# Performance work log

Measured on AMD Instinct MI355X. Metric: run time of the kernel, lower is better.

Reference implementation:

```python
import jax, jax.numpy as jnp
import numpy as np
from jax import lax

NSTEPS = 7
BN_EPS = 1e-5


def setup_inputs() -> dict:
    key = jax.random.key(0)
    ks = jax.random.split(key, 7)
    bs, in_ch, h, w, k = 8, 16, 256, 256, 3
    f = jax.random.normal(ks[0], (bs, in_ch, h, w), dtype=jnp.float32)
    vec_w = jax.random.normal(ks[1], (2 * in_ch, in_ch, k, k), dtype=jnp.float32) * 0.1
    vec_b = jax.random.normal(ks[2], (2 * in_ch,), dtype=jnp.float32) * 0.1
    bn_gamma = jnp.ones((2 * in_ch,), dtype=jnp.float32)
    bn_beta = jnp.zeros((2 * in_ch,), dtype=jnp.float32)
    fuse_w = jax.random.normal(ks[3], (in_ch, in_ch, NSTEPS, 1, 1), dtype=jnp.float32) * 0.1
    fuse_b = jax.random.normal(ks[4], (in_ch,), dtype=jnp.float32) * 0.1
    return {"f": f, "vec_w": vec_w, "vec_b": vec_b, "bn_gamma": bn_gamma,
            "bn_beta": bn_beta, "fuse_w": fuse_w, "fuse_b": fuse_b}


def _bilinear_sample(src, py, px):
    """Bilinear sample with zero padding (torch grid_sample align_corners=True).
    src: [N,C,H,W]; py,px: [N,H,W] pixel coordinates (row, col)."""
    N, C, H, W = src.shape
    y0 = jnp.floor(py); x0 = jnp.floor(px)
    wy1 = py - y0; wy0 = 1.0 - wy1
    wx1 = px - x0; wx0 = 1.0 - wx1
    src_flat = src.reshape(N, C, H * W)

    def gather(yi, xi):
        valid = (yi >= 0) & (yi <= H - 1) & (xi >= 0) & (xi <= W - 1)
        yc = jnp.clip(yi, 0, H - 1).astype(jnp.int32)
        xc = jnp.clip(xi, 0, W - 1).astype(jnp.int32)
        idx = (yc * W + xc).reshape(N, 1, H * W)
        vals = jnp.take_along_axis(src_flat, idx, axis=2).reshape(N, C, H, W)
        return vals * valid.astype(src.dtype)[:, None, :, :]

    out = (wy0 * wx0)[:, None] * gather(y0, x0) \
        + (wy0 * wx1)[:, None] * gather(y0, x0 + 1) \
        + (wy1 * wx0)[:, None] * gather(y0 + 1, x0) \
        + (wy1 * wx1)[:, None] * gather(y0 + 1, x0 + 1)
    return out


def _warp(src, flow, grid_y, grid_x):
    # grid + flow in pixel space; original normalizes to [-1,1] then grid_sample
    # un-normalizes with align_corners=True, which is exactly pixel coords grid+flow.
    py = grid_y[None] + flow[:, 0]
    px = grid_x[None] + flow[:, 1]
    return _bilinear_sample(src, py, px)


def reference(f, vec_w, vec_b, bn_gamma, bn_beta, fuse_w, fuse_b):
    bs, in_ch, h, w = f.shape
    # vec_conv + BatchNorm2d (training-mode batch stats, biased variance)
    vec = lax.conv_general_dilated(f, vec_w, (1, 1), [(1, 1), (1, 1)],
                                   dimension_numbers=("NCHW", "OIHW", "NCHW"))
    vec = vec + vec_b[None, :, None, None]
    mean = vec.mean(axis=(0, 2, 3))
    var = vec.var(axis=(0, 2, 3))
    vec = bn_gamma[None, :, None, None] * (vec - mean[None, :, None, None]) \
        * lax.rsqrt(var + BN_EPS)[None, :, None, None] + bn_beta[None, :, None, None]

    c = vec.shape[1]  # = 2*in_ch
    vec = vec.reshape(bs * c // 2, 2, h, w)  # per-channel 2D flow fields

    grid_y, grid_x = jnp.meshgrid(jnp.arange(h, dtype=f.dtype),
                                  jnp.arange(w, dtype=f.dtype), indexing="ij")

    # VecInt: scaling and squaring, keeping every intermediate deformation
    vec = vec * (1.0 / 2 ** NSTEPS)
    deforms = []
    for _ in range(NSTEPS):
        vec = vec + _warp(vec, vec, grid_y, grid_x)
        deforms.append(vec)

    fsrc = f.reshape(bs * in_ch, 1, h, w)
    maps = [_warp(fsrc, d, grid_y, grid_x).reshape(bs, in_ch, h, w) for d in deforms]
    stacked = jnp.stack(maps, axis=2)  # [bs, in_ch, nsteps, h, w]

    # Conv3d with kernel (nsteps,1,1) then squeeze -> per-pixel channel/step mix
    out = jnp.einsum("ocs,bcshw->bohw", fuse_w[:, :, :, 0, 0], stacked)
    out = out + fuse_b[None, :, None, None]
    return out
```

## Files before the change

### kernel.cpp

```cpp
#include <hip/hip_runtime.h>
#include <hip/hip_fp16.h>

#define H 256
#define W 256
#define BS 8
#define IC 16
#define OCH 32
#define NSTEPS 7
#define PLANE (H*W)
#define NFIELDS (BS*IC)
#define BN_N (BS*PLANE)
#define BN_EPS 1e-5f
#define PW 260
#define PSZ (260 * 260)

__global__ void transpose_w_kernel(const float* __restrict__ w,
                                   __half2* __restrict__ wTh) {
    for (int idx = threadIdx.x; idx < IC * 9 * 16; idx += blockDim.x) {
        int rc = idx >> 4;
        int p  = idx & 15;
        float lo = w[(2 * p) * (IC * 9) + rc];
        float hi = w[(2 * p + 1) * (IC * 9) + rc];
        wTh[idx] = __floats2half2_rn(lo, hi);
    }
}

__global__ void guard_zero_kernel(unsigned* __restrict__ bufA,
                                  unsigned* __restrict__ bufB,
                                  unsigned short* __restrict__ f16p) {
    int p = blockIdx.x;
    size_t pb = (size_t)p * PSZ;
    for (int i = threadIdx.x; i < 2064; i += blockDim.x) {
        int row, col;
        if (i < 1040) {
            int r = i / 260;
            row = (r == 0) ? 0 : 256 + r;
            col = i - r * 260;
        } else {
            int j = i - 1040;
            int c = j / 256;
            col = (c == 0) ? 0 : 256 + c;
            row = 1 + (j - c * 256);
        }
        size_t off = pb + (size_t)row * PW + col;
        bufA[off] = 0u;
        bufB[off] = 0u;
        f16p[off] = 0;
    }
}

__global__ __launch_bounds__(256) void dup_kernel(const float* __restrict__ f,
                                                  __half* __restrict__ f16p) {
    int blk = blockIdx.x;
    int p  = blk >> 3;
    int r0 = (blk & 7) * 32;
    const float* fp = f + (size_t)p * PLANE;
    __half* dp = f16p + (size_t)p * PSZ;
    int tx = threadIdx.x;
#pragma unroll 4
    for (int ry = 0; ry < 32; ++ry) {
        int y = r0 + ry;
        dp[(size_t)(y + 1) * PW + tx + 1] = __float2half(fp[(size_t)y * W + tx]);
    }
}

__global__ __launch_bounds__(256, 8) void conv_kernel(
    const float* __restrict__ f, const __half2* __restrict__ wTh,
    const float* __restrict__ vec_b, __half2* __restrict__ vec_out) {
    __shared__ __align__(16) __half sf[16][10][40];

    int blk = blockIdx.x;
    int xcd = blk & 7;
    int i   = blk >> 3;
    int b   = i >> 5;
    int j   = i & 31;
    int ty0 = ((xcd << 2) | (j >> 3)) * 8;
    int tx0 = (j & 7) * 32;
    int tid = threadIdx.x;

    {
        int sic = tid >> 4;
        int st  = tid & 15;
        if (st < 10) {
            int gx0 = tx0 - 4 + 4 * st;
            const float* fpl = f + (size_t)(b * IC + sic) * PLANE;
            bool full = (gx0 >= 0) && (gx0 + 3 < W);
#pragma unroll
            for (int r = 0; r < 10; ++r) {
                int gy = ty0 - 1 + r;
                float4 v = make_float4(0.f, 0.f, 0.f, 0.f);
                if ((unsigned)gy < (unsigned)H) {
                    if (full) {
                        v = *(const float4*)(fpl + (size_t)gy * W + gx0);
                    } else {
                        if ((unsigned)(gx0 + 0) < (unsigned)W) v.x = fpl[(size_t)gy * W + gx0 + 0];
                        if ((unsigned)(gx0 + 1) < (unsigned)W) v.y = fpl[(size_t)gy * W + gx0 + 1];
                        if ((unsigned)(gx0 + 2) < (unsigned)W) v.z = fpl[(size_t)gy * W + gx0 + 2];
                        if ((unsigned)(gx0 + 3) < (unsigned)W) v.w = fpl[(size_t)gy * W + gx0 + 3];
                    }
                }
                union { __half2 h[2]; float2 f2; } u;
                u.h[0] = __floats2half2_rn(v.x, v.y);
                u.h[1] = __floats2half2_rn(v.z, v.w);
                *(float2*)&sf[sic][r][4 * st] = u.f2;
            }
        }
    }

    __half2 acc[16];
#pragma unroll
    for (int p = 0; p < 16; ++p)
        acc[p] = __floats2half2_rn(vec_b[2 * p], vec_b[2 * p + 1]);

    __syncthreads();

    int tyl = tid >> 5, txl = tid & 31;
#pragma unroll 2
    for (int ic = 0; ic < 16; ++ic) {
#pragma unroll
        for (int k = 0; k < 9; ++k) {
            int ky = k / 3, kx = k - ky * 3;
            __half2 fv = __half2half2(sf[ic][tyl + ky][txl + kx + 3]);
            const __half2* wrow = wTh + (ic * 9 + k) * 16;
#pragma unroll
            for (int p = 0; p < 16; ++p)
                acc[p] = __hfma2(fv, wrow[p], acc[p]);
        }
    }

    int y = ty0 + tyl, x = tx0 + txl;
#pragma unroll
    for (int c = 0; c < IC; ++c)
        vec_out[(size_t)(b * IC + c) * PLANE + (size_t)y * W + x] = acc[c];
}

__global__ __launch_bounds__(256) void stats_kernel(
    const __half2* __restrict__ vec, float* __restrict__ stats) {
    int blk   = blockIdx.x;
    int n     = blk >> 4;
    int chunk = blk & 15;
    const float4* p4 = (const float4*)(vec + (size_t)n * PLANE + chunk * 4096);
    int tid = threadIdx.x;

    float s0 = 0.f, s1 = 0.f, q0 = 0.f, q1 = 0.f;
#pragma unroll 2
    for (int i = tid; i < 1024; i += 256) {
        float4 w = p4[i];
        const __half2* hh = (const __half2*)&w;
#pragma unroll
        for (int q = 0; q < 4; ++q) {
            float2 v = __half22float2(hh[q]);
            s0 += v.x; s1 += v.y;
            q0 = fmaf(v.x, v.x, q0);
            q1 = fmaf(v.y, v.y, q1);
        }
    }
#pragma unroll
    for (int off = 32; off > 0; off >>= 1) {
        s0 += __shfl_down(s0, off, 64);
        s1 += __shfl_down(s1, off, 64);
        q0 += __shfl_down(q0, off, 64);
        q1 += __shfl_down(q1, off, 64);
    }
    __shared__ float red[4][4];
    int wave = tid >> 6, lane = tid & 63;
    if (lane == 0) {
        red[wave][0] = s0; red[wave][1] = s1;
        red[wave][2] = q0; red[wave][3] = q1;
    }
    __syncthreads();
    if (tid == 0) {
        float t0 = 0.f, t1 = 0.f, t2 = 0.f, t3 = 0.f;
#pragma unroll
        for (int wv = 0; wv < 4; ++wv) {
            t0 += red[wv][0]; t1 += red[wv][1];
            t2 += red[wv][2]; t3 += red[wv][3];
        }
        int ch0 = 2 * (n & 15);
        atomicAdd(stats + ch0,          t0);
        atomicAdd(stats + ch0 + 1,      t1);
        atomicAdd(stats + 32 + ch0,     t2);
        atomicAdd(stats + 32 + ch0 + 1, t3);
    }
}

__global__ void finalize_kernel(const float* __restrict__ stats,
                                const float* __restrict__ gamma,
                                const float* __restrict__ beta,
                                float* __restrict__ AB) {
    int ch = threadIdx.x;
    if (ch < 2 * IC) {
        const float invN = 1.f / (float)BN_N;
        float mean = stats[ch] * invN;
        float var  = stats[32 + ch] * invN - mean * mean;
        float rs   = rsqrtf(var + BN_EPS);
        float a    = gamma[ch] * rs;
        AB[ch]      = a * (1.f / 128.f);
        AB[32 + ch] = (beta[ch] - a * mean) * (1.f / 128.f);
    }
}

__device__ __forceinline__ void tap_setup(float py, float px,
                                          int* o, float* wt) {
    float ffy = floorf(py), ffx = floorf(px);
    int y0 = (int)ffy, x0 = (int)ffx;
    float wy1 = py - ffy, wy0 = 1.f - wy1;
    float wx1 = px - ffx, wx0 = 1.f - wx1;
    bool vy0 = (unsigned)y0 < (unsigned)H, vy1 = (unsigned)(y0 + 1) < (unsigned)H;
    bool vx0 = (unsigned)x0 < (unsigned)W, vx1 = (unsigned)(x0 + 1) < (unsigned)W;
    int yc0 = min(max(y0, 0), H - 1), yc1 = min(max(y0 + 1, 0), H - 1);
    int xc0 = min(max(x0, 0), W - 1), xc1 = min(max(x0 + 1, 0), W - 1);
    o[0] = yc0 * W + xc0; o[1] = yc0 * W + xc1;
    o[2] = yc1 * W + xc0; o[3] = yc1 * W + xc1;
    wt[0] = (vy0 && vx0) ? wy0 * wx0 : 0.f;
    wt[1] = (vy0 && vx1) ? wy0 * wx1 : 0.f;
    wt[2] = (vy1 && vx0) ? wy1 * wx0 : 0.f;
    wt[3] = (vy1 && vx1) ? wy1 * wx1 : 0.f;
}

__device__ __forceinline__ void tap_fast(float py, float px,
                                         int& o, float* wt) {
    float pyc = fminf(fmaxf(py, -1.f), 256.f);
    float pxc = fminf(fmaxf(px, -1.f), 256.f);
    float fy = floorf(pyc), fx = floorf(pxc);
    int y0 = (int)fy, x0 = (int)fx;
    float wy1 = pyc - fy, wy0 = 1.f - wy1;
    float wx1 = pxc - fx, wx0 = 1.f - wx1;
    o = (y0 + 1) * PW + (x0 + 1);
    wt[0] = wy0 * wx0; wt[1] = wy0 * wx1;
    wt[2] = wy1 * wx0; wt[3] = wy1 * wx1;
}

template <bool FIRST, bool LAST>
__global__ __launch_bounds__(256, 8) void warp_step(
    const __half2* __restrict__ vinRaw, const __half2* __restrict__ vinPad,
    __half2* __restrict__ voutPad, const __half* __restrict__ f16p,
    const float* __restrict__ AB, __half* __restrict__ mvOut) {
    int blk  = blockIdx.x;
    int fld  = blk & 127;
    int band = blk >> 7;
    int c    = fld & 15;
    int tx   = threadIdx.x;
    const __half2* vinR = FIRST ? vinRaw + (size_t)fld * PLANE : nullptr;
    const __half2* vinP = FIRST ? nullptr : vinPad + (size_t)fld * PSZ;
    __half2* voutP = LAST ? nullptr : voutPad + (size_t)fld * PSZ;
    const __half* fp = f16p + (size_t)fld * PSZ;
    __half* mv = mvOut + (size_t)fld * PLANE;

    float a0 = 0.f, b0 = 0.f, a1 = 0.f, b1 = 0.f;
    if (FIRST) {
        a0 = AB[2 * c];     b0 = AB[32 + 2 * c];
        a1 = AB[2 * c + 1]; b1 = AB[32 + 2 * c + 1];
    }

#pragma unroll 4
    for (int r = 0; r < 8; ++r) {
        int h = band * 8 + r;
        int idx_raw = h * W + tx;
        int idx_pad = (h + 1) * PW + tx + 1;
        float ny, nx;
        if (FIRST) {
            float2 vc = __half22float2(vinR[idx_raw]);
            float fy = fmaf(a0, vc.x, b0);
            float fx = fmaf(a1, vc.y, b1);
            int om[4]; float wt[4];
            tap_setup((float)h + fy, (float)tx + fx, om, wt);
            float2 t0 = __half22float2(vinR[om[0]]);
            float2 t1 = __half22float2(vinR[om[1]]);
            float2 t2 = __half22float2(vinR[om[2]]);
            float2 t3 = __half22float2(vinR[om[3]]);
            float Sy = wt[0] * t0.x + wt[1] * t1.x + wt[2] * t2.x + wt[3] * t3.x;
            float Sx = wt[0] * t0.y + wt[1] * t1.y + wt[2] * t2.y + wt[3] * t3.y;
            float Ws = wt[0] + wt[1] + wt[2] + wt[3];
            ny = fy + fmaf(a0, Sy, b0 * Ws);
            nx = fx + fmaf(a1, Sx, b1 * Ws);
        } else {
            float2 vc = __half22float2(vinP[idx_pad]);
            float fy = vc.x, fx = vc.y;
            int ob; float wt[4];
            tap_fast((float)h + fy, (float)tx + fx, ob, wt);
            union { float2 f2; __half2 hh[2]; } top, bot;
            top.f2 = *reinterpret_cast<const float2*>(vinP + ob);
            bot.f2 = *reinterpret_cast<const float2*>(vinP + ob + PW);
            float2 t0 = __half22float2(top.hh[0]);
            float2 t1 = __half22float2(top.hh[1]);
            float2 t2 = __half22float2(bot.hh[0]);
            float2 t3 = __half22float2(bot.hh[1]);
            ny = fy + wt[0] * t0.x + wt[1] * t1.x + wt[2] * t2.x + wt[3] * t3.x;
            nx = fx + wt[0] * t0.y + wt[1] * t1.y + wt[2] * t2.y + wt[3] * t3.y;
        }
        if (!LAST)
            voutP[idx_pad] = __float22half2_rn(make_float2(ny, nx));
        int pb; float pw[4];
        tap_fast((float)h + ny, (float)tx + nx, pb, pw);
        union { float f; __half2 h2; } r0u, r1u;
        r0u.f = *reinterpret_cast<const float*>(fp + pb);
        r1u.f = *reinterpret_cast<const float*>(fp + pb + PW);
        float2 g0 = __half22float2(r0u.h2);
        float2 g1 = __half22float2(r1u.h2);
        float m = pw[0] * g0.x + pw[1] * g0.y + pw[2] * g1.x + pw[3] * g1.y;
        mv[idx_raw] = __float2half(m);
    }
}

__global__ __launch_bounds__(256) void mix_kernel(
    const __half* __restrict__ mvs,
    const __half* __restrict__ mv6,
    const float* __restrict__ fw, const float* __restrict__ fb,
    float* __restrict__ out) {
    int blk = blockIdx.x;
    int b   = blk >> 8;
    int h   = blk & 255;
    int tx  = threadIdx.x;
    int idx = h * W + tx;

    float acc[IC];
#pragma unroll
    for (int o = 0; o < IC; ++o) acc[o] = fb[o];

#pragma unroll 2
    for (int s = 0; s < NSTEPS; ++s) {
        const __half* base = (s < NSTEPS - 1)
            ? mvs + (size_t)s * NFIELDS * PLANE : mv6;
        const __half* pbm = base + (size_t)b * IC * PLANE + idx;
        __half m[IC];
#pragma unroll
        for (int c = 0; c < IC; ++c)
            m[c] = pbm[(size_t)c * PLANE];
        const float* fws = fw + s;
#pragma unroll
        for (int c = 0; c < IC; ++c) {
            float mf = __half2float(m[c]);
#pragma unroll
            for (int o = 0; o < IC; ++o)
                acc[o] = fmaf(fws[(o * IC + c) * NSTEPS], mf, acc[o]);
        }
    }

#pragma unroll
    for (int o = 0; o < IC; ++o)
        out[(size_t)(b * IC + o) * PLANE + idx] = acc[o];
}

extern "C" void kernel_launch(void* const* d_in, const int* in_sizes, int n_in,
                              void* d_out, int out_size, void* d_ws,
                              size_t ws_size, hipStream_t stream) {
    const float* f      = (const float*)d_in[0];
    const float* vec_w  = (const float*)d_in[1];
    const float* vec_b  = (const float*)d_in[2];
    const float* gamma  = (const float*)d_in[3];
    const float* beta   = (const float*)d_in[4];
    const float* fuse_w = (const float*)d_in[5];
    const float* fuse_b = (const float*)d_in[6];
    float* out = (float*)d_out;

    char* ws = (char*)d_ws;
    const size_t rawB   = (size_t)NFIELDS * PLANE * sizeof(__half2);
    const size_t padB2  = (size_t)NFIELDS * PSZ * sizeof(__half2);
    const size_t padB1  = (size_t)NFIELDS * PSZ * sizeof(__half);
    const size_t smallB = 16384;
    __half2* bufRaw = (__half2*)ws;
    __half2* bufA   = (__half2*)(ws + rawB);
    __half2* bufB   = (__half2*)(ws + rawB + padB2);
    __half*  f16p   = (__half*)(ws + rawB + 2 * padB2);
    char*    smallp = ws + rawB + 2 * padB2 + padB1;
    __half2* wTh    = (__half2*)smallp;
    float*   stats  = (float*)(smallp + 10240);
    float*   AB     = (float*)(smallp + 10240 + 256);
    __half*  mvs    = (__half*)(smallp + smallB);

    hipMemsetAsync(stats, 0, 64 * sizeof(float), stream);
    transpose_w_kernel<<<1, 512, 0, stream>>>(vec_w, wTh);
    guard_zero_kernel<<<NFIELDS, 256, 0, stream>>>(
        (unsigned*)bufA, (unsigned*)bufB, (unsigned short*)f16p);
    dup_kernel<<<NFIELDS * 8, 256, 0, stream>>>(f, f16p);
    conv_kernel<<<2048, 256, 0, stream>>>(f, wTh, vec_b, bufRaw);
    stats_kernel<<<NFIELDS * 16, 256, 0, stream>>>(bufRaw, stats);
    finalize_kernel<<<1, 64, 0, stream>>>(stats, gamma, beta, AB);

    for (int s = 0; s < NSTEPS; ++s) {
        const __half2* vinPad = (s & 1) ? bufA : bufB;
        __half2*       voutP  = (s & 1) ? bufB : bufA;
        __half* mvP = (s < NSTEPS - 1) ? mvs + (size_t)s * NFIELDS * PLANE
                                       : (__half*)bufRaw;
        if (s == 0)
            warp_step<true, false><<<4096, 256, 0, stream>>>(
                bufRaw, (const __half2*)nullptr, bufA, f16p, AB, mvP);
        else if (s < NSTEPS - 1)
            warp_step<false, false><<<4096, 256, 0, stream>>>(
                (const __half2*)nullptr, vinPad, voutP, f16p, AB, mvP);
        else
            warp_step<false, true><<<4096, 256, 0, stream>>>(
                (const __half2*)nullptr, vinPad, (__half2*)nullptr, f16p,
                AB, mvP);
    }
    mix_kernel<<<2048, 256, 0, stream>>>(
        mvs, (const __half*)bufRaw, fuse_w, fuse_b, out);
}
```

Baseline: 469.9 us.

## Stage row window of flow and source in LDS for warp steps

For steps after the first, each block first loads a 17-row window of the padded flow field and the fp16 source image into shared memory. The bilinear gathers then read from LDS when the sampled row falls inside the window and fall back to global memory otherwise. The aim is to replace scattered global or L2 gather traffic with LDS reads. In exchange it adds a cooperative load and a barrier, uses about 26KB of LDS per block with launch bounds lowered to 4, and preloads rows that may never be used.

```diff
diff --git a/kernel.cpp b/kernel.cpp
--- a/kernel.cpp
+++ b/kernel.cpp
@@ -13,6 +13,7 @@
 #define BN_EPS 1e-5f
 #define PW 260
 #define PSZ (260 * 260)
+#define SROWS 17
 
 __global__ void transpose_w_kernel(const float* __restrict__ w,
                                    __half2* __restrict__ wTh) {
@@ -231,66 +232,56 @@
     wt[2] = wy1 * wx0; wt[3] = wy1 * wx1;
 }
 
-template <bool FIRST, bool LAST>
-__global__ __launch_bounds__(256, 8) void warp_step(
-    const __half2* __restrict__ vinRaw, const __half2* __restrict__ vinPad,
-    __half2* __restrict__ voutPad, const __half* __restrict__ f16p,
-    const float* __restrict__ AB, __half* __restrict__ mvOut) {
+__device__ __forceinline__ void tap_fast2(float py, float px,
+                                          int& r0, int& c0, float* wt) {
+    float pyc = fminf(fmaxf(py, -1.f), 256.f);
+    float pxc = fminf(fmaxf(px, -1.f), 256.f);
+    float fy = floorf(pyc), fx = floorf(pxc);
+    int y0 = (int)fy, x0 = (int)fx;
+    float wy1 = pyc - fy, wy0 = 1.f - wy1;
+    float wx1 = pxc - fx, wx0 = 1.f - wx1;
+    r0 = y0 + 1; c0 = x0 + 1;
+    wt[0] = wy0 * wx0; wt[1] = wy0 * wx1;
+    wt[2] = wy1 * wx0; wt[3] = wy1 * wx1;
+}
+
+__global__ __launch_bounds__(256, 8) void warp_step_first(
+    const __half2* __restrict__ vinRaw, __half2* __restrict__ voutPad,
+    const __half* __restrict__ f16p, const float* __restrict__ AB,
+    __half* __restrict__ mvOut) {
     int blk  = blockIdx.x;
     int fld  = blk & 127;
     int band = blk >> 7;
     int c    = fld & 15;
     int tx   = threadIdx.x;
-    const __half2* vinR = FIRST ? vinRaw + (size_t)fld * PLANE : nullptr;
-    const __half2* vinP = FIRST ? nullptr : vinPad + (size_t)fld * PSZ;
-    __half2* voutP = LAST ? nullptr : voutPad + (size_t)fld * PSZ;
+    const __half2* vinR = vinRaw + (size_t)fld * PLANE;
+    __half2* voutP = voutPad + (size_t)fld * PSZ;
     const __half* fp = f16p + (size_t)fld * PSZ;
     __half* mv = mvOut + (size_t)fld * PLANE;
 
-    float a0 = 0.f, b0 = 0.f, a1 = 0.f, b1 = 0.f;
-    if (FIRST) {
-        a0 = AB[2 * c];     b0 = AB[32 + 2 * c];
-        a1 = AB[2 * c + 1]; b1 = AB[32 + 2 * c + 1];
-    }
+    float a0 = AB[2 * c],     b0 = AB[32 + 2 * c];
+    float a1 = AB[2 * c + 1], b1 = AB[32 + 2 * c + 1];
 
 #pragma unroll 4
     for (int r = 0; r < 8; ++r) {
         int h = band * 8 + r;
         int idx_raw = h * W + tx;
         int idx_pad = (h + 1) * PW + tx + 1;
-        float ny, nx;
-        if (FIRST) {
-            float2 vc = __half22float2(vinR[idx_raw]);
-            float fy = fmaf(a0, vc.x, b0);
-            float fx = fmaf(a1, vc.y, b1);
-            int om[4]; float wt[4];
-            tap_setup((float)h + fy, (float)tx + fx, om, wt);
-            float2 t0 = __half22float2(vinR[om[0]]);
-            float2 t1 = __half22float2(vinR[om[1]]);
-            float2 t2 = __half22float2(vinR[om[2]]);
-            float2 t3 = __half22float2(vinR[om[3]]);
-            float Sy = wt[0] * t0.x + wt[1] * t1.x + wt[2] * t2.x + wt[3] * t3.x;
-            float Sx = wt[0] * t0.y + wt[1] * t1.y + wt[2] * t2.y + wt[3] * t3.y;
-            float Ws = wt[0] + wt[1] + wt[2] + wt[3];
-            ny = fy + fmaf(a0, Sy, b0 * Ws);
-            nx = fx + fmaf(a1, Sx, b1 * Ws);
-        } else {
-            float2 vc = __half22float2(vinP[idx_pad]);
-            float fy = vc.x, fx = vc.y;
-            int ob; float wt[4];
-            tap_fast((float)h + fy, (float)tx + fx, ob, wt);
-            union { float2 f2; __half2 hh[2]; } top, bot;
-            top.f2 = *reinterpret_cast<const float2*>(vinP + ob);
-            bot.f2 = *reinterpret_cast<const float2*>(vinP + ob + PW);
-            float2 t0 = __half22float2(top.hh[0]);
-            float2 t1 = __half22float2(top.hh[1]);
-            float2 t2 = __half22float2(bot.hh[0]);
-            float2 t3 = __half22float2(bot.hh[1]);
-            ny = fy + wt[0] * t0.x + wt[1] * t1.x + wt[2] * t2.x + wt[3] * t3.x;
-            nx = fx + wt[0] * t0.y + wt[1] * t1.y + wt[2] * t2.y + wt[3] * t3.y;
-        }
-        if (!LAST)
-            voutP[idx_pad] = __float22half2_rn(make_float2(ny, nx));
+        float2 vc = __half22float2(vinR[idx_raw]);
+        float fy = fmaf(a0, vc.x, b0);
+        float fx = fmaf(a1, vc.y, b1);
+        int om[4]; float wt[4];
+        tap_setup((float)h + fy, (float)tx + fx, om, wt);
+        float2 t0 = __half22float2(vinR[om[0]]);
+        float2 t1 = __half22float2(vinR[om[1]]);
+        float2 t2 = __half22float2(vinR[om[2]]);
+        float2 t3 = __half22float2(vinR[om[3]]);
+        float Sy = wt[0] * t0.x + wt[1] * t1.x + wt[2] * t2.x + wt[3] * t3.x;
+        float Sx = wt[0] * t0.y + wt[1] * t1.y + wt[2] * t2.y + wt[3] * t3.y;
+        float Ws = wt[0] + wt[1] + wt[2] + wt[3];
+        float ny = fy + fmaf(a0, Sy, b0 * Ws);
+        float nx = fx + fmaf(a1, Sx, b1 * Ws);
+        voutP[idx_pad] = __float22half2_rn(make_float2(ny, nx));
         int pb; float pw[4];
         tap_fast((float)h + ny, (float)tx + nx, pb, pw);
         union { float f; __half2 h2; } r0u, r1u;
@@ -299,6 +290,95 @@
         float2 g0 = __half22float2(r0u.h2);
         float2 g1 = __half22float2(r1u.h2);
         float m = pw[0] * g0.x + pw[1] * g0.y + pw[2] * g1.x + pw[3] * g1.y;
+        mv[idx_raw] = __float2half(m);
+    }
+}
+
+template <bool LAST>
+__global__ __launch_bounds__(256, 4) void warp_step_lds(
+    const __half2* __restrict__ vinPad, __half2* __restrict__ voutPad,
+    const __half* __restrict__ f16p, __half* __restrict__ mvOut) {
+    __shared__ __half2 svin[SROWS][260];
+    __shared__ __half  sf16[SROWS][260];
+
+    int blk  = blockIdx.x;
+    int fld  = blk & 127;
+    int band = blk >> 7;
+    int tx   = threadIdx.x;
+    const __half2* vinP = vinPad + (size_t)fld * PSZ;
+    __half2* voutP = LAST ? nullptr : voutPad + (size_t)fld * PSZ;
+    const __half* fp = f16p + (size_t)fld * PSZ;
+    __half* mv = mvOut + (size_t)fld * PLANE;
+
+    const int P0  = band * 8 + 1;
+    const int Wlo = P0 - 4;
+
+#pragma unroll
+    for (int r = 0; r < SROWS; ++r) {
+        int pr = Wlo + r;
+        if ((unsigned)pr <= 259u) {
+            const __half2* src  = vinP + (size_t)pr * PW;
+            const __half*  srcf = fp + (size_t)pr * PW;
+            svin[r][tx] = src[tx];
+            sf16[r][tx] = srcf[tx];
+            if (tx < 4) {
+                svin[r][256 + tx] = src[256 + tx];
+                sf16[r][256 + tx] = srcf[256 + tx];
+            }
+        }
+    }
+    __syncthreads();
+
+#pragma unroll 4
+    for (int rr = 0; rr < 8; ++rr) {
+        int h = band * 8 + rr;
+        int idx_raw = h * W + tx;
+        int idx_pad = (h + 1) * PW + tx + 1;
+        float2 vc = __half22float2(svin[rr + 4][tx + 1]);
+        float fy = vc.x, fx = vc.y;
+        int r0, c0; float wt[4];
+        tap_fast2((float)h + fy, (float)tx + fx, r0, c0, wt);
+        float2 t0, t1, t2, t3;
+        if ((unsigned)(r0 - Wlo) <= (unsigned)(SROWS - 2)) {
+            int lr = r0 - Wlo;
+            t0 = __half22float2(svin[lr][c0]);
+            t1 = __half22float2(svin[lr][c0 + 1]);
+            t2 = __half22float2(svin[lr + 1][c0]);
+            t3 = __half22float2(svin[lr + 1][c0 + 1]);
+        } else {
+            const __half2* gp = vinP + (size_t)r0 * PW + c0;
+            union { float2 f2; __half2 hh[2]; } top, bot;
+            top.f2 = *reinterpret_cast<const float2*>(gp);
+            bot.f2 = *reinterpret_cast<const float2*>(gp + PW);
+            t0 = __half22float2(top.hh[0]);
+            t1 = __half22float2(top.hh[1]);
+            t2 = __half22float2(bot.hh[0]);
+            t3 = __half22float2(bot.hh[1]);
+        }
+        float ny = fy + wt[0] * t0.x + wt[1] * t1.x + wt[2] * t2.x + wt[3] * t3.x;
+        float nx = fx + wt[0] * t0.y + wt[1] * t1.y + wt[2] * t2.y + wt[3] * t3.y;
+        if (!LAST)
+            voutP[idx_pad] = __float22half2_rn(make_float2(ny, nx));
+
+        int rf, cf; float pw[4];
+        tap_fast2((float)h + ny, (float)tx + nx, rf, cf, pw);
+        float m;
+        if ((unsigned)(rf - Wlo) <= (unsigned)(SROWS - 2)) {
+            int lr = rf - Wlo;
+            float g00 = __half2float(sf16[lr][cf]);
+            float g01 = __half2float(sf16[lr][cf + 1]);
+            float g10 = __half2float(sf16[lr + 1][cf]);
+            float g11 = __half2float(sf16[lr + 1][cf + 1]);
+            m = pw[0] * g00 + pw[1] * g01 + pw[2] * g10 + pw[3] * g11;
+        } else {
+            const __half* gp = fp + (size_t)rf * PW + cf;
+            union { float f; __half2 h2; } r0u, r1u;
+            r0u.f = *reinterpret_cast<const float*>(gp);
+            r1u.f = *reinterpret_cast<const float*>(gp + PW);
+            float2 g0 = __half22float2(r0u.h2);
+            float2 g1 = __half22float2(r1u.h2);
+            m = pw[0] * g0.x + pw[1] * g0.y + pw[2] * g1.x + pw[3] * g1.y;
+        }
         mv[idx_raw] = __float2half(m);
     }
 }
@@ -384,15 +464,14 @@
         __half* mvP = (s < NSTEPS - 1) ? mvs + (size_t)s * NFIELDS * PLANE
                                        : (__half*)bufRaw;
         if (s == 0)
-            warp_step<true, false><<<4096, 256, 0, stream>>>(
-                bufRaw, (const __half2*)nullptr, bufA, f16p, AB, mvP);
+            warp_step_first<<<4096, 256, 0, stream>>>(
+                bufRaw, bufA, f16p, AB, mvP);
         else if (s < NSTEPS - 1)
-            warp_step<false, false><<<4096, 256, 0, stream>>>(
-                (const __half2*)nullptr, vinPad, voutP, f16p, AB, mvP);
+            warp_step_lds<false><<<4096, 256, 0, stream>>>(
+                vinPad, voutP, f16p, mvP);
         else
-            warp_step<false, true><<<4096, 256, 0, stream>>>(
-                (const __half2*)nullptr, vinPad, (__half2*)nullptr, f16p,
-                AB, mvP);
+            warp_step_lds<true><<<4096, 256, 0, stream>>>(
+                vinPad, (__half2*)nullptr, f16p, mvP);
     }
     mix_kernel<<<2048, 256, 0, stream>>>(
         mvs, (const __half*)bufRaw, fuse_w, fuse_b, out);
```

Measured after the change: 644.1 us. +37.1%, slower.
